# Performance work log

Hardware: AMD Instinct MI355X
Metric: run time of the kernel (lower is better)

## Reference

```python
import jax, jax.numpy as jnp
import numpy as np

B, T, D = 2, 2048, 2048
N_HEADS, N_KV, HEAD_DIM = 8, 4, 256
S_CACHE = 2048
WINDOW = 512
SOFT_CAP = 50.0
ROPE_TS = 10000
ROPE_PROP = 1.0
EPS = 1e-6
NEG_INF = -2.3819763e38


def setup_inputs() -> dict:
    key = jax.random.key(0)
    ks = jax.random.split(key, 6)
    x = jax.random.normal(ks[0], (B, T, D), dtype=jnp.float32)
    wq = jax.random.normal(ks[1], (D, N_HEADS * HEAD_DIM), dtype=jnp.float32) * (D ** -0.5)
    wk = jax.random.normal(ks[2], (D, N_KV * HEAD_DIM), dtype=jnp.float32) * (D ** -0.5)
    wv = jax.random.normal(ks[3], (D, N_KV * HEAD_DIM), dtype=jnp.float32) * (D ** -0.5)
    wo = jax.random.normal(ks[4], (N_HEADS * HEAD_DIM, D), dtype=jnp.float32) * ((N_HEADS * HEAD_DIM) ** -0.5)
    return {
        'x': x,
        'segment_pos': jnp.broadcast_to(jnp.arange(T, dtype=jnp.int32), (B, T)),
        'cur_ind': 0,
        'wq': wq, 'wk': wk, 'wv': wv, 'wo': wo,
        'q_norm_scale': jnp.zeros((HEAD_DIM,), jnp.float32),
        'k_norm_scale': jnp.zeros((HEAD_DIM,), jnp.float32),
        'k_cache': jnp.zeros((B, S_CACHE, N_KV, HEAD_DIM), jnp.float32),
        'v_cache': jnp.zeros((B, S_CACHE, N_KV, HEAD_DIM), jnp.float32),
    }


def _rms_norm(x, scale, eps=EPS):
    # Gemma4RMSNorm: fp32 norm, (1 + scale) offset
    xf = x.astype(jnp.float32)
    n = xf * jax.lax.rsqrt(jnp.mean(jnp.square(xf), -1, keepdims=True) + eps)
    return (n * (1.0 + scale)).astype(x.dtype)


def _apply_rope(x, pos, max_timescale=ROPE_TS, proportion=ROPE_PROP):
    # x: [B, T, n, H]; pos: [B, T]. Partial RoPE on first proportion*H dims.
    H = x.shape[-1]
    rope_dim = int(H * proportion)
    half = rope_dim // 2
    frac = jnp.arange(half, dtype=jnp.float32) / half
    timescale = jnp.asarray(max_timescale, jnp.float32) ** frac  # [half]
    sinusoid = pos.astype(jnp.float32)[..., None] / timescale    # [B, T, half]
    sin = jnp.sin(sinusoid)[:, :, None, :]
    cos = jnp.cos(sinusoid)[:, :, None, :]
    x_rope, x_pass = x[..., :rope_dim], x[..., rope_dim:]
    x1, x2 = x_rope[..., :half], x_rope[..., half:]
    rotated = jnp.concatenate([x1 * cos - x2 * sin, x2 * cos + x1 * sin], axis=-1)
    return jnp.concatenate([rotated, x_pass], axis=-1).astype(x.dtype)


def reference(x, segment_pos, cur_ind, wq, wk, wv, wo, q_norm_scale, k_norm_scale, k_cache, v_cache):
    b, t, _ = x.shape
    g = N_HEADS // N_KV  # GQA group size

    q = (x @ wq).reshape(b, t, N_HEADS, HEAD_DIM)
    k = (x @ wk).reshape(b, t, N_KV, HEAD_DIM)
    v = (x @ wv).reshape(b, t, N_KV, HEAD_DIM)

    # QK-norm (per-head RMSNorm) then RoPE
    q = _rms_norm(q, q_norm_scale)
    k = _rms_norm(k, k_norm_scale)
    q = _apply_rope(q, segment_pos)
    k = _apply_rope(k, segment_pos)

    # KV-cache scatter write at cur_ind
    idx = jnp.asarray(cur_ind, jnp.int32)
    k_cache = jax.lax.dynamic_update_slice(k_cache, k, (0, idx, 0, 0))
    v_cache = jax.lax.dynamic_update_slice(v_cache, v, (0, idx, 0, 0))

    # Attention logits over full cache: [b, kv, g, t, s]
    qg = q.reshape(b, t, N_KV, g, HEAD_DIM) * (HEAD_DIM ** -0.5)
    logits = jnp.einsum('btkgh,bskh->bkgts', qg, k_cache)
    logits = SOFT_CAP * jnp.tanh(logits / SOFT_CAP)

    # Causal + sliding-window mask from absolute positions
    q_pos = segment_pos[:, :, None]                              # [b, t, 1]
    k_pos = jnp.arange(S_CACHE, dtype=jnp.int32)[None, None, :]  # [1, 1, s]
    mask = (k_pos <= q_pos) & (q_pos - k_pos < WINDOW)           # [b, t, s]
    logits = jnp.where(mask[:, None, None, :, :], logits, NEG_INF)

    probs = jax.nn.softmax(logits, axis=-1)
    attn = jnp.einsum('bkgts,bskh->btkgh', probs, v_cache).reshape(b, t, N_HEADS * HEAD_DIM)
    return attn @ wo
```

## Files before the change

kernel.cpp:

```cpp
#include <hip/hip_runtime.h>

#define T_SEQ 2048
#define NHEADS 8
#define NKV 4
#define HD 256
#define WIN 512

typedef __bf16 bf16x8 __attribute__((ext_vector_type(8)));
typedef float f32x4 __attribute__((ext_vector_type(4)));

__device__ __forceinline__ float bf2f(unsigned short u) {
    return __uint_as_float(((unsigned int)u) << 16);
}
__device__ __forceinline__ unsigned short f2bf(float f) {
    unsigned int u = __float_as_uint(f);
    u += 0x7fffu + ((u >> 16) & 1u);
    return (unsigned short)(u >> 16);
}

#define GLOAD_LDS16(gptr, lptr)                                            \
    __builtin_amdgcn_global_load_lds(                                      \
        (const __attribute__((address_space(1))) unsigned int*)(gptr),     \
        (__attribute__((address_space(3))) unsigned int*)(lptr), 16, 0, 0)

__global__ void detect_dtype(const unsigned short* __restrict__ x, int* flag) {
    int tid = threadIdx.x;
    int cnt = 0;
    for (int i = 0; i < 64; ++i) {
        unsigned short u = x[2 * (tid * 64 + i)];
        int e = (u >> 7) & 0xFF;
        cnt += (e >= 100 && e <= 140) ? 1 : 0;
    }
    #pragma unroll
    for (int o = 32; o >= 1; o >>= 1) cnt += __shfl_xor(cnt, o);
    if (tid == 0) *flag = (cnt > 2048) ? 1 : 0;
}

__global__ __launch_bounds__(256) void convert_to_bf16(
    const void* __restrict__ src, unsigned short* __restrict__ dst,
    const int* __restrict__ flag, int n)
{
    int i = (blockIdx.x * 256 + threadIdx.x) * 8;
    if (i >= n) return;
    if (*flag) {
        *(uint4*)&dst[i] = *(const uint4*)((const unsigned short*)src + i);
    } else {
        const float* s = (const float*)src + i;
        unsigned short v[8];
        #pragma unroll
        for (int j = 0; j < 8; ++j) v[j] = f2bf(s[j]);
        *(uint4*)&dst[i] = *(uint4*)v;
    }
}

__global__ __launch_bounds__(256) void transpose_cvt(
    const void* __restrict__ src, unsigned short* __restrict__ dst,
    const int* __restrict__ flag, int R, int C)
{
    __shared__ unsigned short tile[32][33];
    const int t = threadIdx.x;
    const int c = t & 31, r8 = t >> 5;
    const int bx = blockIdx.x, by = blockIdx.y;
    const int isb = *flag;
    #pragma unroll
    for (int i = 0; i < 4; ++i) {
        int r = r8 + i * 8;
        size_t idx = (size_t)(by * 32 + r) * C + bx * 32 + c;
        tile[r][c] = isb ? ((const unsigned short*)src)[idx]
                         : f2bf(((const float*)src)[idx]);
    }
    __syncthreads();
    #pragma unroll
    for (int i = 0; i < 4; ++i) {
        int r = r8 + i * 8;
        dst[(size_t)(bx * 32 + r) * R + by * 32 + c] = tile[c][r];
    }
}

__global__ __launch_bounds__(256) void transpose_qkv_w(
    const void* __restrict__ wq, const void* __restrict__ wk,
    const void* __restrict__ wv, unsigned short* __restrict__ dst,
    const int* __restrict__ flag)
{
    __shared__ unsigned short tile[32][33];
    const int t = threadIdx.x;
    const int c = t & 31, r8 = t >> 5;
    const int bx = blockIdx.x, by = blockIdx.y;
    const void* src; int C, rowoff, cb;
    if (bx < 64)      { src = wq; C = 2048; rowoff = 0;    cb = bx; }
    else if (bx < 96) { src = wk; C = 1024; rowoff = 2048; cb = bx - 64; }
    else              { src = wv; C = 1024; rowoff = 3072; cb = bx - 96; }
    const int isb = *flag;
    #pragma unroll
    for (int i = 0; i < 4; ++i) {
        int r = r8 + i * 8;
        size_t idx = (size_t)(by * 32 + r) * C + cb * 32 + c;
        tile[r][c] = isb ? ((const unsigned short*)src)[idx]
                         : f2bf(((const float*)src)[idx]);
    }
    __syncthreads();
    #pragma unroll
    for (int i = 0; i < 4; ++i) {
        int r = r8 + i * 8;
        dst[(size_t)(rowoff + cb * 32 + r) * 2048 + by * 32 + c] = tile[c][r];
    }
}

__global__ __launch_bounds__(256) void gemm_bf16(
    const unsigned short* __restrict__ A,
    const unsigned short* __restrict__ Bt,
    void* __restrict__ C,
    int M, int Ntot, int K, int n_base,
    const int* __restrict__ flag, int force_bf16)
{
    __shared__ __align__(16) unsigned short As[2][128 * 32];
    __shared__ __align__(16) unsigned short Bs[2][128 * 32];
    const int tid = threadIdx.x;
    const int n0 = blockIdx.x * 128;
    const int m0 = blockIdx.y * 128;
    const int wave = tid >> 6;
    const int lane = tid & 63;
    const int wm = (wave >> 1) * 64;
    const int wn = (wave & 1) * 64;
    const int quad = lane >> 4;
    const int l16 = lane & 15;
    const int obf = force_bf16 | *flag;

    const int ch0 = tid, ch1 = tid + 256;
    const unsigned short* a0 = A  + (size_t)(m0 + (ch0 >> 2)) * K + (ch0 & 3) * 8;
    const unsigned short* a1 = A  + (size_t)(m0 + (ch1 >> 2)) * K + (ch1 & 3) * 8;
    const unsigned short* b0 = Bt + (size_t)(n0 + (ch0 >> 2)) * K + (ch0 & 3) * 8;
    const unsigned short* b1 = Bt + (size_t)(n0 + (ch1 >> 2)) * K + (ch1 & 3) * 8;

    f32x4 acc[4][4];
    #pragma unroll
    for (int i = 0; i < 4; ++i)
        #pragma unroll
        for (int j = 0; j < 4; ++j)
            acc[i][j] = f32x4{0.f, 0.f, 0.f, 0.f};

    const int NT = K >> 5;

#define STAGE_G(buf, tile_)                              \
    do { int _o = (tile_) * 32;                          \
        GLOAD_LDS16(a0 + _o, &As[buf][ch0 * 8]);         \
        GLOAD_LDS16(b0 + _o, &Bs[buf][ch0 * 8]);         \
        GLOAD_LDS16(a1 + _o, &As[buf][ch1 * 8]);         \
        GLOAD_LDS16(b1 + _o, &Bs[buf][ch1 * 8]);         \
    } while (0)

    STAGE_G(0, 0);
    STAGE_G(1, 1);

    for (int t = 0; t < NT; ++t) {
        if (t < NT - 1) asm volatile("s_waitcnt vmcnt(4)" ::: "memory");
        else            asm volatile("s_waitcnt vmcnt(0)" ::: "memory");
        __builtin_amdgcn_s_barrier();
        __builtin_amdgcn_sched_barrier(0);

        const int cb = t & 1;
        bf16x8 af[4], bfr[4];
        #pragma unroll
        for (int mi = 0; mi < 4; ++mi)
            af[mi] = *(const bf16x8*)&As[cb][(wm + mi * 16 + l16) * 32 + quad * 8];
        #pragma unroll
        for (int ni = 0; ni < 4; ++ni)
            bfr[ni] = *(const bf16x8*)&Bs[cb][(wn + ni * 16 + l16) * 32 + quad * 8];
        #pragma unroll
        for (int mi = 0; mi < 4; ++mi)
            #pragma unroll
            for (int ni = 0; ni < 4; ++ni)
                acc[mi][ni] = __builtin_amdgcn_mfma_f32_16x16x32_bf16(
                    af[mi], bfr[ni], acc[mi][ni], 0, 0, 0);

        __builtin_amdgcn_sched_barrier(0);
        __builtin_amdgcn_s_barrier();
        if (t + 2 < NT) STAGE_G(cb, t + 2);
    }
#undef STAGE_G

    #pragma unroll
    for (int mi = 0; mi < 4; ++mi)
        #pragma unroll
        for (int ni = 0; ni < 4; ++ni)
            #pragma unroll
            for (int r = 0; r < 4; ++r) {
                int row = m0 + wm + mi * 16 + quad * 4 + r;
                int col = n_base + n0 + wn + ni * 16 + l16;
                size_t idx = (size_t)row * Ntot + col;
                if (obf) ((unsigned short*)C)[idx] = f2bf(acc[mi][ni][r]);
                else     ((float*)C)[idx]          = acc[mi][ni][r];
            }
}

__global__ __launch_bounds__(256) void finalize_qk(
    unsigned short* __restrict__ qkv,
    const int* __restrict__ segment_pos,
    const void* __restrict__ qs_raw,
    const void* __restrict__ ks_raw,
    const int* __restrict__ flag)
{
    const int w = blockIdx.x * 4 + (threadIdx.x >> 6);
    const int lane = threadIdx.x & 63;
    const int b = w / (T_SEQ * 12);
    const int rem = w % (T_SEQ * 12);
    const int t = rem / 12;
    const int slot = rem % 12;
    const bool isq = slot < 8;
    const int col0 = isq ? slot * 256 : 2048 + (slot - 8) * 256;
    unsigned short* p = qkv + (size_t)(b * T_SEQ + t) * 4096 + col0;
    const int isb = *flag;

    float e[4];
    #pragma unroll
    for (int j = 0; j < 4; ++j) e[j] = bf2f(p[lane + 64 * j]);
    float ss = e[0] * e[0] + e[1] * e[1] + e[2] * e[2] + e[3] * e[3];
    #pragma unroll
    for (int o = 32; o >= 1; o >>= 1) ss += __shfl_xor(ss, o);
    const float rn = rsqrtf(ss * (1.0f / 256.0f) + 1e-6f);
    const void* scp = isq ? qs_raw : ks_raw;
    float nrm[4];
    #pragma unroll
    for (int j = 0; j < 4; ++j) {
        float sc = isb ? bf2f(((const unsigned short*)scp)[lane + 64 * j])
                       : ((const float*)scp)[lane + 64 * j];
        nrm[j] = e[j] * rn * (1.0f + sc);
    }

    const int pos = segment_pos[b * T_SEQ + t];
    #pragma unroll
    for (int pp = 0; pp < 2; ++pp) {
        const int i = lane + 64 * pp;
        const float inv_ts = __expf((float)i * -0.07195578415606293f);
        float s, c;
        __sincosf((float)pos * inv_ts, &s, &c);
        const float x1 = nrm[pp], x2 = nrm[pp + 2];
        p[i]       = f2bf(x1 * c - x2 * s);
        p[i + 128] = f2bf(x2 * c + x1 * s);
    }
}

__global__ __launch_bounds__(256) void build_vt(
    const unsigned short* __restrict__ qkv, unsigned short* __restrict__ vt)
{
    __shared__ unsigned short tile[32][33];
    const int bkv = blockIdx.z;
    const int b = bkv >> 2, kv = bkv & 3;
    const int s0 = blockIdx.x * 32, d0 = blockIdx.y * 32;
    const int c = threadIdx.x & 31, r8 = threadIdx.x >> 5;
    #pragma unroll
    for (int i = 0; i < 4; ++i) {
        int r = r8 + i * 8;
        tile[r][c] = qkv[(size_t)(b * T_SEQ + s0 + r) * 4096 + 3072 + kv * 256 + d0 + c];
    }
    __syncthreads();
    #pragma unroll
    for (int i = 0; i < 4; ++i) {
        int r = r8 + i * 8;
        vt[((size_t)bkv * 256 + d0 + r) * T_SEQ + s0 + c] = tile[c][r];
    }
}

#define PSTR 80
__global__ __launch_bounds__(256, 2) void attn_mfma(
    const unsigned short* __restrict__ qkv,
    const unsigned short* __restrict__ vt,
    unsigned short* __restrict__ out)
{
    __shared__ __align__(16) unsigned short SMEM[16384 + 16384 + 4 * 16 * PSTR];
    unsigned short* K_lds  = SMEM;
    unsigned short* VT_lds = SMEM + 16384;

    const int tid = threadIdx.x;
    const int wave = tid >> 6, lane = tid & 63;
    const int l16 = lane & 15, quad = lane >> 4;
    const int sw = l16 & 7;
    const int bkv = blockIdx.x & 7;
    const int qt  = blockIdx.x >> 3;
    const int b = bkv >> 2, kvh = bkv & 3;
    const int t0 = qt * 32;
    const int h = kvh * 2 + (wave >> 1);
    const int woff = (wave & 1) * 16;
    const int tq = t0 + woff + l16;
    unsigned short* P_lds = SMEM + 32768 + wave * 16 * PSTR;

    bf16x8 qf[8];
    {
        const unsigned short* qp =
            qkv + (size_t)(b * T_SEQ + tq) * 4096 + h * 256 + quad * 8;
        #pragma unroll
        for (int c = 0; c < 8; ++c) qf[c] = *(const bf16x8*)(qp + 32 * c);
    }

    f32x4 o[16];
    #pragma unroll
    for (int nt = 0; nt < 16; ++nt) o[nt] = f32x4{0.f, 0.f, 0.f, 0.f};
    float l_run = 0.f;

    int s_lo = t0 - (WIN - 1); if (s_lo < 0) s_lo = 0;
    const int s_base = s_lo & ~63;
    const int s_last = t0 + 31;
    const int tqmin = t0 + woff;
    const int tqmax = tqmin + 15;
    const int wlo   = tqmin - (WIN - 1);
    const size_t kgbase = (size_t)b * T_SEQ * 4096 + 2048 + kvh * 256;
    const size_t vgbase = (size_t)bkv * 256 * T_SEQ;

    for (int sb = s_base; sb <= s_last; sb += 64) {
        __syncthreads();

        #pragma unroll
        for (int i = 0; i < 8; ++i) {
            int ch = tid + 256 * i;
            int row = ch >> 5, e8 = ch & 31;
            GLOAD_LDS16(&qkv[kgbase + (size_t)(sb + row) * 4096
                             + ((e8 ^ (row & 7)) * 8)],
                        &K_lds[ch * 8]);
        }
        #pragma unroll
        for (int i = 0; i < 8; ++i) {
            int ch = tid + 256 * i;
            int dr = ch >> 3, e8 = ch & 7;
            GLOAD_LDS16(&vt[vgbase + (size_t)dr * T_SEQ + sb
                            + ((e8 ^ (dr & 7)) * 8)],
                        &VT_lds[ch * 8]);
        }
        __syncthreads();

        if (sb > tqmax || sb + 63 < wlo) continue;

        f32x4 st[4];
        #pragma unroll
        for (int mt = 0; mt < 4; ++mt) st[mt] = f32x4{0.f, 0.f, 0.f, 0.f};
        __builtin_amdgcn_s_setprio(1);
        #pragma unroll
        for (int c = 0; c < 8; ++c) {
            bf16x8 kf[4];
            #pragma unroll
            for (int mt = 0; mt < 4; ++mt)
                kf[mt] = *(const bf16x8*)&K_lds[(mt * 16 + l16) * 256 + (((4 * c + quad) ^ sw) * 8)];
            #pragma unroll
            for (int mt = 0; mt < 4; ++mt)
                st[mt] = __builtin_amdgcn_mfma_f32_16x16x32_bf16(kf[mt], qf[c], st[mt], 0, 0, 0);
        }
        __builtin_amdgcn_s_setprio(0);

        #pragma unroll
        for (int mt = 0; mt < 4; ++mt)
            #pragma unroll
            for (int r = 0; r < 4; ++r) {
                int sp = sb + mt * 16 + quad * 4 + r;
                float e2 = __expf(st[mt][r] * 0.0025f);
                float p = __expf(20.0f - 100.0f / (e2 + 1.0f));
                bool valid = (sp <= tq) && (tq - sp < WIN);
                p = valid ? p : 0.0f;
                l_run += p;
                P_lds[l16 * PSTR + mt * 16 + quad * 4 + r] = f2bf(p);
            }

        #pragma unroll
        for (int c = 0; c < 2; ++c) {
            bf16x8 pf = *(const bf16x8*)&P_lds[l16 * PSTR + 32 * c + quad * 8];
            __builtin_amdgcn_s_setprio(1);
            #pragma unroll
            for (int nt = 0; nt < 16; ++nt) {
                bf16x8 vf = *(const bf16x8*)&VT_lds[(nt * 16 + l16) * 64 + (((4 * c + quad) ^ sw) * 8)];
                o[nt] = __builtin_amdgcn_mfma_f32_16x16x32_bf16(pf, vf, o[nt], 0, 0, 0);
            }
            __builtin_amdgcn_s_setprio(0);
        }
    }

    l_run += __shfl_xor(l_run, 16);
    l_run += __shfl_xor(l_run, 32);
    float linv[4];
    #pragma unroll
    for (int r = 0; r < 4; ++r) linv[r] = 1.0f / __shfl(l_run, quad * 4 + r);

    __syncthreads();
    unsigned short* W = SMEM + wave * (16 * 264);
    #pragma unroll
    for (int nt = 0; nt < 16; ++nt)
        #pragma unroll
        for (int r = 0; r < 4; ++r)
            W[(quad * 4 + r) * 264 + nt * 16 + l16] = f2bf(o[nt][r] * linv[r]);
    const int lr = lane >> 2, lc = (lane & 3) * 64;
    unsigned short* ob = out + (size_t)(b * T_SEQ + t0 + woff + lr) * 2048 + h * 256 + lc;
    #pragma unroll
    for (int j = 0; j < 8; ++j)
        *(uint4*)(ob + j * 8) = *(const uint4*)&W[lr * 264 + lc + j * 8];
}

extern "C" void kernel_launch(void* const* d_in, const int* in_sizes, int n_in,
                              void* d_out, int out_size, void* d_ws, size_t ws_size,
                              hipStream_t stream) {
    const void* x   = d_in[0];
    const int*  sp  = (const int*)d_in[1];
    const void* wq  = d_in[3];
    const void* wk  = d_in[4];
    const void* wv  = d_in[5];
    const void* wo  = d_in[6];
    const void* qsc = d_in[7];
    const void* ksc = d_in[8];

    unsigned short* ws = (unsigned short*)d_ws;
    int*            flag = (int*)ws;
    unsigned short* qkv  = (unsigned short*)d_out;
    dim3 blk(256);

    const size_t NEED = (size_t)(2048 + 8388608 + 8388608) * sizeof(unsigned short);

    detect_dtype<<<1, 64, 0, stream>>>((const unsigned short*)x, flag);

    if (ws_size >= NEED) {
        unsigned short* xhat = ws + 2048;
        unsigned short* wT   = xhat + (size_t)4096 * 2048;
        unsigned short* abuf = xhat;
        unsigned short* vtb  = wT;
        unsigned short* woT  = wT + (size_t)2048 * 2048;

        convert_to_bf16<<<4096, blk, 0, stream>>>(x, xhat, flag, 4096 * 2048);

        transpose_qkv_w<<<dim3(128, 64), blk, 0, stream>>>(wq, wk, wv, wT, flag);

        gemm_bf16<<<dim3(32, 32), blk, 0, stream>>>(xhat, wT, qkv,
                                                    4096, 4096, 2048, 0, flag, 1);

        finalize_qk<<<12288, blk, 0, stream>>>(qkv, sp, qsc, ksc, flag);

        build_vt<<<dim3(64, 8, 8), blk, 0, stream>>>(qkv, vtb);
        attn_mfma<<<512, blk, 0, stream>>>(qkv, vtb, abuf);

        transpose_cvt<<<dim3(64, 64), blk, 0, stream>>>(wo, woT, flag, 2048, 2048);
        gemm_bf16<<<dim3(16, 32), blk, 0, stream>>>(abuf, woT, d_out,
                                                    4096, 2048, 2048, 0, flag, 0);
    } else {
        unsigned short* reg1 = ws + 2048;
        unsigned short* reg2 = reg1 + (size_t)4096 * 2048;
        unsigned short* xhat = reg1;
        unsigned short* abuf = reg1;

        convert_to_bf16<<<4096, blk, 0, stream>>>(x, xhat, flag, 4096 * 2048);

        transpose_cvt<<<dim3(64, 64), blk, 0, stream>>>(wq, reg2, flag, 2048, 2048);
        gemm_bf16<<<dim3(16, 32), blk, 0, stream>>>(xhat, reg2, qkv,
                                                    4096, 4096, 2048, 0, flag, 1);
        transpose_cvt<<<dim3(32, 64), blk, 0, stream>>>(wk, reg2,                     flag, 2048, 1024);
        transpose_cvt<<<dim3(32, 64), blk, 0, stream>>>(wv, reg2 + (size_t)1024*2048, flag, 2048, 1024);
        gemm_bf16<<<dim3(16, 32), blk, 0, stream>>>(xhat, reg2, qkv,
                                                    4096, 4096, 2048, 2048, flag, 1);

        finalize_qk<<<12288, blk, 0, stream>>>(qkv, sp, qsc, ksc, flag);

        build_vt<<<dim3(64, 8, 8), blk, 0, stream>>>(qkv, reg2);
        attn_mfma<<<512, blk, 0, stream>>>(qkv, reg2, abuf);

        transpose_cvt<<<dim3(64, 64), blk, 0, stream>>>(wo, reg2, flag, 2048, 2048);
        gemm_bf16<<<dim3(16, 32), blk, 0, stream>>>(abuf, reg2, d_out,
                                                    4096, 2048, 2048, 0, flag, 0);
    }
}
```

Before: 380.7 us.

## Use 256x256 tiled GEMM with XOR-swizzled LDS for QKV projection

Adds a 512-thread GEMM kernel with 256x256 output tiles and a K-step of 64. It double-buffers LDS through direct global-to-LDS loads, XOR-swizzles the LDS columns to avoid bank conflicts, remaps blocks in a swizzled order, and raises wave priority around the MFMA bursts. The QKV projection now uses this kernel to get more data reuse per tile. The old gemm_bf16 loses its double buffering and becomes a simple single-buffer loop, which slows the output projection that still calls it. The new kernel uses a large LDS footprint, so fewer blocks fit per CU.

```diff
diff --git a/kernel.cpp b/kernel.cpp
--- a/kernel.cpp
+++ b/kernel.cpp
@@ -113,8 +113,8 @@
     int M, int Ntot, int K, int n_base,
     const int* __restrict__ flag, int force_bf16)
 {
-    __shared__ __align__(16) unsigned short As[2][128 * 32];
-    __shared__ __align__(16) unsigned short Bs[2][128 * 32];
+    __shared__ __align__(16) unsigned short As[128 * 32];
+    __shared__ __align__(16) unsigned short Bs[128 * 32];
     const int tid = threadIdx.x;
     const int n0 = blockIdx.x * 128;
     const int m0 = blockIdx.y * 128;
@@ -126,12 +126,6 @@
     const int l16 = lane & 15;
     const int obf = force_bf16 | *flag;
 
-    const int ch0 = tid, ch1 = tid + 256;
-    const unsigned short* a0 = A  + (size_t)(m0 + (ch0 >> 2)) * K + (ch0 & 3) * 8;
-    const unsigned short* a1 = A  + (size_t)(m0 + (ch1 >> 2)) * K + (ch1 & 3) * 8;
-    const unsigned short* b0 = Bt + (size_t)(n0 + (ch0 >> 2)) * K + (ch0 & 3) * 8;
-    const unsigned short* b1 = Bt + (size_t)(n0 + (ch1 >> 2)) * K + (ch1 & 3) * 8;
-
     f32x4 acc[4][4];
     #pragma unroll
     for (int i = 0; i < 4; ++i)
@@ -139,45 +133,31 @@
         for (int j = 0; j < 4; ++j)
             acc[i][j] = f32x4{0.f, 0.f, 0.f, 0.f};
 
-    const int NT = K >> 5;
-
-#define STAGE_G(buf, tile_)                              \
-    do { int _o = (tile_) * 32;                          \
-        GLOAD_LDS16(a0 + _o, &As[buf][ch0 * 8]);         \
-        GLOAD_LDS16(b0 + _o, &Bs[buf][ch0 * 8]);         \
-        GLOAD_LDS16(a1 + _o, &As[buf][ch1 * 8]);         \
-        GLOAD_LDS16(b1 + _o, &Bs[buf][ch1 * 8]);         \
-    } while (0)
-
-    STAGE_G(0, 0);
-    STAGE_G(1, 1);
-
-    for (int t = 0; t < NT; ++t) {
-        if (t < NT - 1) asm volatile("s_waitcnt vmcnt(4)" ::: "memory");
-        else            asm volatile("s_waitcnt vmcnt(0)" ::: "memory");
-        __builtin_amdgcn_s_barrier();
-        __builtin_amdgcn_sched_barrier(0);
-
-        const int cb = t & 1;
+    for (int kk = 0; kk < K; kk += 32) {
+        #pragma unroll
+        for (int i = 0; i < 2; ++i) {
+            int ch = tid + i * 256;
+            int row = ch >> 2;
+            int ko = (ch & 3) * 8;
+            GLOAD_LDS16(&A[(size_t)(m0 + row) * K + kk + ko],  &As[ch * 8]);
+            GLOAD_LDS16(&Bt[(size_t)(n0 + row) * K + kk + ko], &Bs[ch * 8]);
+        }
+        __syncthreads();
         bf16x8 af[4], bfr[4];
         #pragma unroll
         for (int mi = 0; mi < 4; ++mi)
-            af[mi] = *(const bf16x8*)&As[cb][(wm + mi * 16 + l16) * 32 + quad * 8];
+            af[mi] = *(const bf16x8*)&As[(wm + mi * 16 + l16) * 32 + quad * 8];
         #pragma unroll
         for (int ni = 0; ni < 4; ++ni)
-            bfr[ni] = *(const bf16x8*)&Bs[cb][(wn + ni * 16 + l16) * 32 + quad * 8];
+            bfr[ni] = *(const bf16x8*)&Bs[(wn + ni * 16 + l16) * 32 + quad * 8];
         #pragma unroll
         for (int mi = 0; mi < 4; ++mi)
             #pragma unroll
             for (int ni = 0; ni < 4; ++ni)
                 acc[mi][ni] = __builtin_amdgcn_mfma_f32_16x16x32_bf16(
                     af[mi], bfr[ni], acc[mi][ni], 0, 0, 0);
-
-        __builtin_amdgcn_sched_barrier(0);
-        __builtin_amdgcn_s_barrier();
-        if (t + 2 < NT) STAGE_G(cb, t + 2);
-    }
-#undef STAGE_G
+        __syncthreads();
+    }
 
     #pragma unroll
     for (int mi = 0; mi < 4; ++mi)
@@ -187,6 +167,162 @@
             for (int r = 0; r < 4; ++r) {
                 int row = m0 + wm + mi * 16 + quad * 4 + r;
                 int col = n_base + n0 + wn + ni * 16 + l16;
+                size_t idx = (size_t)row * Ntot + col;
+                if (obf) ((unsigned short*)C)[idx] = f2bf(acc[mi][ni][r]);
+                else     ((float*)C)[idx]          = acc[mi][ni][r];
+            }
+}
+
+__global__ __launch_bounds__(512, 2) void gemm256_bf16(
+    const unsigned short* __restrict__ A,
+    const unsigned short* __restrict__ Bt,
+    void* __restrict__ C,
+    int M, int Ntot, int K, int n_base, int gx,
+    const int* __restrict__ flag, int force_bf16)
+{
+    __shared__ __align__(16) unsigned short A_lds[2][256 * 64];
+    __shared__ __align__(16) unsigned short B_lds[2][256 * 64];
+
+    const int tid = threadIdx.x;
+    const int cpx = gridDim.x >> 3;
+    const int swzb = (blockIdx.x & 7) * cpx + (blockIdx.x >> 3);
+    const int bx = swzb % gx, by = swzb / gx;
+    const int n0 = bx * 256, m0 = by * 256;
+
+    const int wave = tid >> 6, lane = tid & 63;
+    const int wr = wave >> 2, wc = wave & 3;
+    const int quad = lane >> 4, l16 = lane & 15;
+    const int sw7 = l16 & 7;
+    const int obf = force_bf16 | *flag;
+
+    const int r0 = tid >> 3;
+    const int chs = ((tid & 7) ^ (r0 & 7)) * 8;
+    const unsigned short* Ab = A  + (size_t)(m0 + r0) * K + chs;
+    const unsigned short* Bb = Bt + (size_t)(n0 + r0) * K + chs;
+
+    f32x4 acc[8][4];
+    #pragma unroll
+    for (int i = 0; i < 8; ++i)
+        #pragma unroll
+        for (int j = 0; j < 4; ++j)
+            acc[i][j] = f32x4{0.f, 0.f, 0.f, 0.f};
+
+    const int NT = K >> 6;
+
+#define STAGE256(buf_, kt_)                                               \
+    do {                                                                  \
+        _Pragma("unroll")                                                 \
+        for (int j = 0; j < 4; ++j) {                                     \
+            GLOAD_LDS16(Ab + (size_t)(64 * j) * K + (kt_) * 64,           \
+                        &A_lds[buf_][(tid + 512 * j) * 8]);               \
+            GLOAD_LDS16(Bb + (size_t)(64 * j) * K + (kt_) * 64,           \
+                        &B_lds[buf_][(tid + 512 * j) * 8]);               \
+        }                                                                 \
+    } while (0)
+
+    STAGE256(0, 0);
+    __syncthreads();
+
+    for (int t = 0; t < NT; ++t) {
+        const int cb = t & 1;
+        if (t + 1 < NT) STAGE256(cb ^ 1, t + 1);
+
+        const unsigned short* Ac = A_lds[cb];
+        const unsigned short* Bc = B_lds[cb];
+        bf16x8 a4[4][2], b2[2][2];
+
+        #pragma unroll
+        for (int mi = 0; mi < 4; ++mi)
+            #pragma unroll
+            for (int ks = 0; ks < 2; ++ks)
+                a4[mi][ks] = *(const bf16x8*)&Ac[(wr * 128 + mi * 16 + l16) * 64
+                                                + (((ks * 4 + quad) ^ sw7) * 8)];
+        #pragma unroll
+        for (int ni = 0; ni < 2; ++ni)
+            #pragma unroll
+            for (int ks = 0; ks < 2; ++ks)
+                b2[ni][ks] = *(const bf16x8*)&Bc[(wc * 64 + ni * 16 + l16) * 64
+                                                + (((ks * 4 + quad) ^ sw7) * 8)];
+        __builtin_amdgcn_s_setprio(1);
+        #pragma unroll
+        for (int mi = 0; mi < 4; ++mi)
+            #pragma unroll
+            for (int ni = 0; ni < 2; ++ni)
+                #pragma unroll
+                for (int ks = 0; ks < 2; ++ks)
+                    acc[mi][ni] = __builtin_amdgcn_mfma_f32_16x16x32_bf16(
+                        a4[mi][ks], b2[ni][ks], acc[mi][ni], 0, 0, 0);
+        __builtin_amdgcn_s_setprio(0);
+
+        #pragma unroll
+        for (int ni = 0; ni < 2; ++ni)
+            #pragma unroll
+            for (int ks = 0; ks < 2; ++ks)
+                b2[ni][ks] = *(const bf16x8*)&Bc[(wc * 64 + (ni + 2) * 16 + l16) * 64
+                                                + (((ks * 4 + quad) ^ sw7) * 8)];
+        __builtin_amdgcn_s_setprio(1);
+        #pragma unroll
+        for (int mi = 0; mi < 4; ++mi)
+            #pragma unroll
+            for (int ni = 0; ni < 2; ++ni)
+                #pragma unroll
+                for (int ks = 0; ks < 2; ++ks)
+                    acc[mi][ni + 2] = __builtin_amdgcn_mfma_f32_16x16x32_bf16(
+                        a4[mi][ks], b2[ni][ks], acc[mi][ni + 2], 0, 0, 0);
+        __builtin_amdgcn_s_setprio(0);
+
+        #pragma unroll
+        for (int mi = 0; mi < 4; ++mi)
+            #pragma unroll
+            for (int ks = 0; ks < 2; ++ks)
+                a4[mi][ks] = *(const bf16x8*)&Ac[(wr * 128 + (mi + 4) * 16 + l16) * 64
+                                                + (((ks * 4 + quad) ^ sw7) * 8)];
+        #pragma unroll
+        for (int ni = 0; ni < 2; ++ni)
+            #pragma unroll
+            for (int ks = 0; ks < 2; ++ks)
+                b2[ni][ks] = *(const bf16x8*)&Bc[(wc * 64 + ni * 16 + l16) * 64
+                                                + (((ks * 4 + quad) ^ sw7) * 8)];
+        __builtin_amdgcn_s_setprio(1);
+        #pragma unroll
+        for (int mi = 0; mi < 4; ++mi)
+            #pragma unroll
+            for (int ni = 0; ni < 2; ++ni)
+                #pragma unroll
+                for (int ks = 0; ks < 2; ++ks)
+                    acc[mi + 4][ni] = __builtin_amdgcn_mfma_f32_16x16x32_bf16(
+                        a4[mi][ks], b2[ni][ks], acc[mi + 4][ni], 0, 0, 0);
+        __builtin_amdgcn_s_setprio(0);
+
+        #pragma unroll
+        for (int ni = 0; ni < 2; ++ni)
+            #pragma unroll
+            for (int ks = 0; ks < 2; ++ks)
+                b2[ni][ks] = *(const bf16x8*)&Bc[(wc * 64 + (ni + 2) * 16 + l16) * 64
+                                                + (((ks * 4 + quad) ^ sw7) * 8)];
+        __builtin_amdgcn_s_setprio(1);
+        #pragma unroll
+        for (int mi = 0; mi < 4; ++mi)
+            #pragma unroll
+            for (int ni = 0; ni < 2; ++ni)
+                #pragma unroll
+                for (int ks = 0; ks < 2; ++ks)
+                    acc[mi + 4][ni + 2] = __builtin_amdgcn_mfma_f32_16x16x32_bf16(
+                        a4[mi][ks], b2[ni][ks], acc[mi + 4][ni + 2], 0, 0, 0);
+        __builtin_amdgcn_s_setprio(0);
+
+        __syncthreads();
+    }
+#undef STAGE256
+
+    #pragma unroll
+    for (int mi = 0; mi < 8; ++mi)
+        #pragma unroll
+        for (int ni = 0; ni < 4; ++ni)
+            #pragma unroll
+            for (int r = 0; r < 4; ++r) {
+                int row = m0 + wr * 128 + mi * 16 + quad * 4 + r;
+                int col = n_base + n0 + wc * 64 + ni * 16 + l16;
                 size_t idx = (size_t)row * Ntot + col;
                 if (obf) ((unsigned short*)C)[idx] = f2bf(acc[mi][ni][r]);
                 else     ((float*)C)[idx]          = acc[mi][ni][r];
@@ -423,8 +559,8 @@
 
         transpose_qkv_w<<<dim3(128, 64), blk, 0, stream>>>(wq, wk, wv, wT, flag);
 
-        gemm_bf16<<<dim3(32, 32), blk, 0, stream>>>(xhat, wT, qkv,
-                                                    4096, 4096, 2048, 0, flag, 1);
+        gemm256_bf16<<<256, 512, 0, stream>>>(xhat, wT, qkv,
+                                              4096, 4096, 2048, 0, 16, flag, 1);
 
         finalize_qk<<<12288, blk, 0, stream>>>(qkv, sp, qsc, ksc, flag);
 
```

Result: faster. 362.1 us (-4.9%).

## Add 256x256 tiled GEMM with swizzled LDS and interleaved pipeline for projections

Applied to the files above, without the earlier changes.

Adds a new 512-thread GEMM kernel with 256x256 output tiles, K-step 64, XOR-swizzled LDS layout, double buffering with staged half-tile loads interleaved between MFMA quarters, and block-index swizzling for L2 locality. It replaces the 128x128 GEMM for the QKV and output projections on the main path. The goal is more reuse per LDS load and fewer bank conflicts. In exchange, only 256 and 128 blocks are launched, which may underfill the GPU's CUs, and register pressure rises. The old gemm_bf16, still used on the fallback path, loses its double buffering in favour of a simpler single-buffered loop.

```diff
diff --git a/kernel.cpp b/kernel.cpp
--- a/kernel.cpp
+++ b/kernel.cpp
@@ -113,8 +113,8 @@
     int M, int Ntot, int K, int n_base,
     const int* __restrict__ flag, int force_bf16)
 {
-    __shared__ __align__(16) unsigned short As[2][128 * 32];
-    __shared__ __align__(16) unsigned short Bs[2][128 * 32];
+    __shared__ __align__(16) unsigned short As[128 * 32];
+    __shared__ __align__(16) unsigned short Bs[128 * 32];
     const int tid = threadIdx.x;
     const int n0 = blockIdx.x * 128;
     const int m0 = blockIdx.y * 128;
@@ -126,12 +126,6 @@
     const int l16 = lane & 15;
     const int obf = force_bf16 | *flag;
 
-    const int ch0 = tid, ch1 = tid + 256;
-    const unsigned short* a0 = A  + (size_t)(m0 + (ch0 >> 2)) * K + (ch0 & 3) * 8;
-    const unsigned short* a1 = A  + (size_t)(m0 + (ch1 >> 2)) * K + (ch1 & 3) * 8;
-    const unsigned short* b0 = Bt + (size_t)(n0 + (ch0 >> 2)) * K + (ch0 & 3) * 8;
-    const unsigned short* b1 = Bt + (size_t)(n0 + (ch1 >> 2)) * K + (ch1 & 3) * 8;
-
     f32x4 acc[4][4];
     #pragma unroll
     for (int i = 0; i < 4; ++i)
@@ -139,45 +133,31 @@
         for (int j = 0; j < 4; ++j)
             acc[i][j] = f32x4{0.f, 0.f, 0.f, 0.f};
 
-    const int NT = K >> 5;
-
-#define STAGE_G(buf, tile_)                              \
-    do { int _o = (tile_) * 32;                          \
-        GLOAD_LDS16(a0 + _o, &As[buf][ch0 * 8]);         \
-        GLOAD_LDS16(b0 + _o, &Bs[buf][ch0 * 8]);         \
-        GLOAD_LDS16(a1 + _o, &As[buf][ch1 * 8]);         \
-        GLOAD_LDS16(b1 + _o, &Bs[buf][ch1 * 8]);         \
-    } while (0)
-
-    STAGE_G(0, 0);
-    STAGE_G(1, 1);
-
-    for (int t = 0; t < NT; ++t) {
-        if (t < NT - 1) asm volatile("s_waitcnt vmcnt(4)" ::: "memory");
-        else            asm volatile("s_waitcnt vmcnt(0)" ::: "memory");
-        __builtin_amdgcn_s_barrier();
-        __builtin_amdgcn_sched_barrier(0);
-
-        const int cb = t & 1;
+    for (int kk = 0; kk < K; kk += 32) {
+        #pragma unroll
+        for (int i = 0; i < 2; ++i) {
+            int ch = tid + i * 256;
+            int row = ch >> 2;
+            int ko = (ch & 3) * 8;
+            GLOAD_LDS16(&A[(size_t)(m0 + row) * K + kk + ko],  &As[ch * 8]);
+            GLOAD_LDS16(&Bt[(size_t)(n0 + row) * K + kk + ko], &Bs[ch * 8]);
+        }
+        __syncthreads();
         bf16x8 af[4], bfr[4];
         #pragma unroll
         for (int mi = 0; mi < 4; ++mi)
-            af[mi] = *(const bf16x8*)&As[cb][(wm + mi * 16 + l16) * 32 + quad * 8];
+            af[mi] = *(const bf16x8*)&As[(wm + mi * 16 + l16) * 32 + quad * 8];
         #pragma unroll
         for (int ni = 0; ni < 4; ++ni)
-            bfr[ni] = *(const bf16x8*)&Bs[cb][(wn + ni * 16 + l16) * 32 + quad * 8];
+            bfr[ni] = *(const bf16x8*)&Bs[(wn + ni * 16 + l16) * 32 + quad * 8];
         #pragma unroll
         for (int mi = 0; mi < 4; ++mi)
             #pragma unroll
             for (int ni = 0; ni < 4; ++ni)
                 acc[mi][ni] = __builtin_amdgcn_mfma_f32_16x16x32_bf16(
                     af[mi], bfr[ni], acc[mi][ni], 0, 0, 0);
-
-        __builtin_amdgcn_sched_barrier(0);
-        __builtin_amdgcn_s_barrier();
-        if (t + 2 < NT) STAGE_G(cb, t + 2);
-    }
-#undef STAGE_G
+        __syncthreads();
+    }
 
     #pragma unroll
     for (int mi = 0; mi < 4; ++mi)
@@ -187,6 +167,157 @@
             for (int r = 0; r < 4; ++r) {
                 int row = m0 + wm + mi * 16 + quad * 4 + r;
                 int col = n_base + n0 + wn + ni * 16 + l16;
+                size_t idx = (size_t)row * Ntot + col;
+                if (obf) ((unsigned short*)C)[idx] = f2bf(acc[mi][ni][r]);
+                else     ((float*)C)[idx]          = acc[mi][ni][r];
+            }
+}
+
+__global__ __launch_bounds__(512, 2) void gemm256_bf16(
+    const unsigned short* __restrict__ A,
+    const unsigned short* __restrict__ Bt,
+    void* __restrict__ C,
+    int M, int Ntot, int K, int n_base, int gx,
+    const int* __restrict__ flag, int force_bf16)
+{
+    __shared__ __align__(16) unsigned short A_lds[2][256 * 64];
+    __shared__ __align__(16) unsigned short B_lds[2][256 * 64];
+
+    const int tid = threadIdx.x;
+    const int cpx = gridDim.x >> 3;
+    const int swzb = (blockIdx.x & 7) * cpx + (blockIdx.x >> 3);
+    const int bx = swzb % gx, by = swzb / gx;
+    const int n0 = bx * 256, m0 = by * 256;
+
+    const int wave = tid >> 6, lane = tid & 63;
+    const int wr = wave >> 2, wc = wave & 3;
+    const int quad = lane >> 4, l16 = lane & 15;
+    const int sw7 = l16 & 7;
+    const int obf = force_bf16 | *flag;
+
+    const int trow = tid >> 3;
+    const int tg   = tid & 7;
+    const int tsw  = (tg ^ (trow & 7)) * 8;
+
+    f32x4 acc[8][4];
+    #pragma unroll
+    for (int i = 0; i < 8; ++i)
+        #pragma unroll
+        for (int j = 0; j < 4; ++j)
+            acc[i][j] = f32x4{0.f, 0.f, 0.f, 0.f};
+
+    const int NT = K >> 6;
+    const int NI = NT >> 1;
+
+#define STAGE_A(d_, hm_, kt_)                                                  \
+    do { _Pragma("unroll") for (int j = 0; j < 2; ++j) {                       \
+        int r_ = j * 128 + (hm_) * 64 + trow;                                  \
+        GLOAD_LDS16(&A[(size_t)(m0 + r_) * K + (kt_) * 64 + tsw],              \
+                    &A_lds[d_][((hm_) * 128 + j * 64 + trow) * 64 + tg * 8]);  \
+    } } while (0)
+
+#define STAGE_B(d_, hn_, kt_)                                                  \
+    do { _Pragma("unroll") for (int j = 0; j < 2; ++j) {                       \
+        int w2_ = j * 64 + trow;                                               \
+        int r_ = (w2_ >> 5) * 64 + (hn_) * 32 + (w2_ & 31);                    \
+        GLOAD_LDS16(&Bt[(size_t)(n0 + r_) * K + (kt_) * 64 + tsw],             \
+                    &B_lds[d_][((hn_) * 128 + w2_) * 64 + tg * 8]);            \
+    } } while (0)
+
+    bf16x8 a[4][2], b0[2][2], b1[2][2];
+
+#define LDA_H(d_, hm_)                                                         \
+    do { _Pragma("unroll") for (int mi = 0; mi < 4; ++mi)                      \
+         _Pragma("unroll") for (int ks = 0; ks < 2; ++ks)                      \
+            a[mi][ks] = *(const bf16x8*)&A_lds[d_][                            \
+                ((hm_) * 128 + wr * 64 + mi * 16 + l16) * 64                   \
+                + (((ks * 4 + quad) ^ sw7) * 8)]; } while (0)
+
+#define LDB_H(d_, hn_, bb_)                                                    \
+    do { _Pragma("unroll") for (int ni = 0; ni < 2; ++ni)                      \
+         _Pragma("unroll") for (int ks = 0; ks < 2; ++ks)                      \
+            bb_[ni][ks] = *(const bf16x8*)&B_lds[d_][                          \
+                ((hn_) * 128 + wc * 32 + ni * 16 + l16) * 64                   \
+                + (((ks * 4 + quad) ^ sw7) * 8)]; } while (0)
+
+#define MFMAQ(hm_, hn_, bb_)                                                   \
+    do { __builtin_amdgcn_s_setprio(1);                                        \
+         _Pragma("unroll") for (int mi = 0; mi < 4; ++mi)                      \
+         _Pragma("unroll") for (int ni = 0; ni < 2; ++ni)                      \
+         _Pragma("unroll") for (int ks = 0; ks < 2; ++ks)                      \
+            acc[(hm_) * 4 + mi][(hn_) * 2 + ni] =                              \
+                __builtin_amdgcn_mfma_f32_16x16x32_bf16(                       \
+                    a[mi][ks], bb_[ni][ks],                                    \
+                    acc[(hm_) * 4 + mi][(hn_) * 2 + ni], 0, 0, 0);             \
+         __builtin_amdgcn_s_setprio(0); } while (0)
+
+#define BAR() do { __builtin_amdgcn_sched_barrier(0);                          \
+                   __builtin_amdgcn_s_barrier();                               \
+                   __builtin_amdgcn_sched_barrier(0); } while (0)
+#define LGKM0() do { asm volatile("s_waitcnt lgkmcnt(0)" ::: "memory");        \
+                     __builtin_amdgcn_sched_barrier(0); } while (0)
+#define VMC(n_) asm volatile("s_waitcnt vmcnt(" #n_ ")" ::: "memory")
+
+    STAGE_A(0, 0, 0); STAGE_B(0, 0, 0); STAGE_B(0, 1, 0); STAGE_A(0, 1, 0);
+    STAGE_A(1, 0, 1); STAGE_B(1, 0, 1); STAGE_B(1, 1, 1);
+    VMC(6);
+    BAR();
+
+    for (int i = 0; i < NI; ++i) {
+        const int t2 = 2 * i + 2, t3 = 2 * i + 3;
+        const bool s2 = t2 < NT, s3 = t3 < NT;
+
+        LDA_H(0, 0); LDB_H(0, 0, b0);
+        STAGE_A(1, 1, 2 * i + 1);
+        BAR(); LGKM0(); MFMAQ(0, 0, b0);
+        BAR();
+        LDB_H(0, 1, b1);
+        if (s2) STAGE_A(0, 0, t2);
+        BAR(); LGKM0(); MFMAQ(0, 1, b1);
+        BAR();
+        LDA_H(0, 1);
+        if (s2) STAGE_B(0, 0, t2);
+        BAR(); LGKM0(); MFMAQ(1, 1, b1);
+        BAR();
+        if (s2) STAGE_B(0, 1, t2);
+        BAR(); LGKM0(); MFMAQ(1, 0, b0);
+        if (s2) { VMC(6); } else { VMC(0); }
+        BAR();
+        LDA_H(1, 0); LDB_H(1, 0, b0);
+        if (s2) STAGE_A(0, 1, t2);
+        BAR(); LGKM0(); MFMAQ(0, 0, b0);
+        BAR();
+        LDB_H(1, 1, b1);
+        if (s3) STAGE_A(1, 0, t3);
+        BAR(); LGKM0(); MFMAQ(0, 1, b1);
+        BAR();
+        LDA_H(1, 1);
+        if (s3) STAGE_B(1, 0, t3);
+        BAR(); LGKM0(); MFMAQ(1, 1, b1);
+        BAR();
+        if (s3) STAGE_B(1, 1, t3);
+        BAR(); LGKM0(); MFMAQ(1, 0, b0);
+        if (s3) { VMC(6); } else { VMC(0); }
+        BAR();
+    }
+
+#undef STAGE_A
+#undef STAGE_B
+#undef LDA_H
+#undef LDB_H
+#undef MFMAQ
+#undef BAR
+#undef LGKM0
+#undef VMC
+
+    #pragma unroll
+    for (int mi = 0; mi < 8; ++mi)
+        #pragma unroll
+        for (int ni = 0; ni < 4; ++ni)
+            #pragma unroll
+            for (int r = 0; r < 4; ++r) {
+                int row = m0 + wr * 128 + mi * 16 + quad * 4 + r;
+                int col = n_base + n0 + wc * 64 + ni * 16 + l16;
                 size_t idx = (size_t)row * Ntot + col;
                 if (obf) ((unsigned short*)C)[idx] = f2bf(acc[mi][ni][r]);
                 else     ((float*)C)[idx]          = acc[mi][ni][r];
@@ -423,8 +554,8 @@
 
         transpose_qkv_w<<<dim3(128, 64), blk, 0, stream>>>(wq, wk, wv, wT, flag);
 
-        gemm_bf16<<<dim3(32, 32), blk, 0, stream>>>(xhat, wT, qkv,
-                                                    4096, 4096, 2048, 0, flag, 1);
+        gemm256_bf16<<<256, 512, 0, stream>>>(xhat, wT, qkv,
+                                              4096, 4096, 2048, 0, 16, flag, 1);
 
         finalize_qk<<<12288, blk, 0, stream>>>(qkv, sp, qsc, ksc, flag);
 
@@ -432,8 +563,8 @@
         attn_mfma<<<512, blk, 0, stream>>>(qkv, vtb, abuf);
 
         transpose_cvt<<<dim3(64, 64), blk, 0, stream>>>(wo, woT, flag, 2048, 2048);
-        gemm_bf16<<<dim3(16, 32), blk, 0, stream>>>(abuf, woT, d_out,
-                                                    4096, 2048, 2048, 0, flag, 0);
+        gemm256_bf16<<<128, 512, 0, stream>>>(abuf, woT, d_out,
+                                              4096, 2048, 2048, 0, 8, flag, 0);
     } else {
         unsigned short* reg1 = ws + 2048;
         unsigned short* reg2 = reg1 + (size_t)4096 * 2048;
```

Result: faster. 359.1 us (-5.7%).
